# Kernel optimization log

Measured on AMD Instinct MI355X. Metric: run time of the kernel, lower is better.

Reference implementation:

```python
import jax, jax.numpy as jnp
import numpy as np
from jax import lax

B, L, D, H, OM = 16, 512, 2048, 512, 5


def _lstm(seq, wih, whh, bih, bhh):
    # seq: [T, B, F]; PyTorch gate order i, f, g, o
    Hh = whh.shape[1]
    Bb = seq.shape[1]
    def step(carry, xt):
        h, c = carry
        g = xt @ wih.T + h @ whh.T + bih + bhh
        i, f, gg, o = jnp.split(g, 4, axis=-1)
        c = jax.nn.sigmoid(f) * c + jax.nn.sigmoid(i) * jnp.tanh(gg)
        h = jax.nn.sigmoid(o) * jnp.tanh(c)
        return (h, c), h
    z = jnp.zeros((Bb, Hh), seq.dtype)
    _, hs = lax.scan(step, (z, z), seq)
    return hs  # [T, B, Hh]


def setup_inputs() -> dict:
    key = jax.random.key(0)
    ks = jax.random.split(key, 17)
    s = 0.02
    f32 = jnp.float32
    inp = {
        "x": jax.random.normal(ks[0], (B, L, D), f32),
        "wb": jax.random.normal(ks[1], (H, D, OM), f32) * s,
        "bb": jax.random.normal(ks[2], (H,), f32) * s,
        "wa": jax.random.normal(ks[3], (H, D, OM), f32) * s,
        "ba": jax.random.normal(ks[4], (H,), f32) * s,
        "wr": jax.random.normal(ks[5], (H, D, 2 * OM), f32) * s,
        "br": jax.random.normal(ks[6], (H,), f32) * s,
        "wih_f": jax.random.normal(ks[7], (4 * H, H + 1), f32) * s,
        "whh_f": jax.random.normal(ks[8], (4 * H, H), f32) * s,
        "bih_f": jax.random.normal(ks[9], (4 * H,), f32) * s,
        "bhh_f": jax.random.normal(ks[10], (4 * H,), f32) * s,
        "wih_r": jax.random.normal(ks[11], (4 * H, H + 1), f32) * s,
        "whh_r": jax.random.normal(ks[12], (4 * H, H), f32) * s,
        "bih_r": jax.random.normal(ks[13], (4 * H,), f32) * s,
        "bhh_r": jax.random.normal(ks[14], (4 * H,), f32) * s,
        "wfc": jax.random.normal(ks[15], (1, 2 * H), f32) * s,
        "bfc": jax.random.normal(ks[16], (1,), f32) * s,
    }
    return inp


def reference(x, wb, bb, wa, ba, wr, br, wih_f, whh_f, bih_f, bhh_f,
              wih_r, whh_r, bih_r, bhh_r, wfc, bfc):
    om = OM
    xc = jnp.transpose(x, (0, 2, 1))  # [B, D, L]
    conv = lambda w, b: lax.conv_general_dilated(
        xc, w, (1,), 'VALID', dimension_numbers=('NCH', 'OIH', 'NCH')) + b[None, :, None]
    cb = conv(wb, bb)  # [B, H, L-om+1]
    ca = conv(wa, ba)  # [B, H, L-om+1]
    cr = conv(wr, br)  # [B, H, L-2om+1]
    T = x.shape[1] - 2 * om  # number of centers c in [om, L-om)
    d_before = cb[:, :, 0:T]          # window [c-om, c) == conv output c-om
    d_after = ca[:, :, om:om + T]     # window [c, c+om) == conv output c
    vts_d = jnp.sum(d_before * d_after, axis=1, keepdims=True)  # [B, 1, T]
    vts_r = cr[:, :, 0:T]             # full window; pool over length-1 is identity
    vts_seq = jnp.concatenate([vts_r, vts_d], axis=1)  # [B, H+1, T]
    seq = jnp.transpose(vts_seq, (2, 0, 1))  # [T, B, H+1]
    hs_f = _lstm(seq, wih_f, whh_f, bih_f, bhh_f)
    hs_r = _lstm(seq[::-1], wih_r, whh_r, bih_r, bhh_r)[::-1]
    h = jnp.concatenate([hs_f, hs_r], axis=-1)  # [T, B, 2H]
    logits = jnp.einsum('tbh,h->tb', h, wfc[0]) + bfc[0]
    return jax.nn.sigmoid(jnp.transpose(logits))  # [B, T]
```

## Files before the change

kernel.cpp:

```cpp
#include <hip/hip_runtime.h>
#include <hip/hip_bf16.h>

typedef short v8s __attribute__((ext_vector_type(8)));
typedef float v4f __attribute__((ext_vector_type(4)));
typedef unsigned int u32;
typedef unsigned short u16;
typedef unsigned long long u64;

__device__ __forceinline__ u16 f2bf(float f) {
    union { float f; u32 u; } x; x.f = f;
    u32 r = x.u + 0x7fffu + ((x.u >> 16) & 1u);
    return (u16)(r >> 16);
}
__device__ __forceinline__ float bf2f(u16 s) {
    union { u32 u; float f; } x; x.u = ((u32)s) << 16;
    return x.f;
}
__device__ __forceinline__ float sigmoidf_(float x) { return 1.f / (1.f + __expf(-x)); }
__device__ __forceinline__ float tanh_fast(float x) {
    float t = fminf(fmaxf(x, -15.f), 15.f);
    float e = __expf(2.f * t);
    return (e - 1.f) / (e + 1.f);
}

__global__ __launch_bounds__(256) void xbf_kernel(const float* __restrict__ x, u16* __restrict__ xbf, int n) {
    int i = (blockIdx.x * 256 + threadIdx.x) * 4;
    if (i + 3 < n) {
        float4 v = *(const float4*)(x + i);
        u16* d = xbf + i;
        d[0] = f2bf(v.x); d[1] = f2bf(v.y); d[2] = f2bf(v.z); d[3] = f2bf(v.w);
    }
}

__global__ __launch_bounds__(256) void packw_kernel(const float* __restrict__ wb, const float* __restrict__ wa,
                                                    const float* __restrict__ wr, u16* __restrict__ W1, u16* __restrict__ W2) {
    long idx = (long)blockIdx.x * 256 + threadIdx.x;
    int which = idx >= (1024L * 10240) ? 1 : 0;
    long rem = idx - (long)which * 1024 * 10240;
    int n = (int)(rem / 10240);
    int kap = (int)(rem % 10240);
    int tap = kap >> 11, d = kap & 2047;
    float v;
    if (n < 512) v = which ? wa[(long)n * 10240 + d * 5 + tap] : wb[(long)n * 10240 + d * 5 + tap];
    else         v = wr[(long)(n - 512) * 20480 + d * 10 + tap + (which ? 5 : 0)];
    (which ? W2 : W1)[rem] = f2bf(v);
}

__global__ __launch_bounds__(256) void packwih_kernel(const float* __restrict__ wf, const float* __restrict__ wr,
                                                      u16* __restrict__ Bp) {
    int idx = blockIdx.x * 256 + threadIdx.x;
    int n = idx / 576, kap = idx % 576;
    int dir = n >> 11, g = n & 2047;
    const float* src = dir ? wr : wf;
    float v = (kap < 513) ? src[(long)g * 513 + kap] : 0.f;
    Bp[idx] = f2bf(v);
}

__global__ __launch_bounds__(256) void packwhh_kernel(const float* __restrict__ whf, const float* __restrict__ whr,
                                                      u16* __restrict__ W) {
    int idx = blockIdx.x * 256 + threadIdx.x;
    int dir = idx >> 20;
    float v = dir ? whr[idx & 1048575] : whf[idx];
    W[idx] = f2bf(v);
}

__global__ __launch_bounds__(256) void misc_kernel(const float* __restrict__ bihf, const float* __restrict__ bhhf,
                                                   const float* __restrict__ bihr, const float* __restrict__ bhhr,
                                                   float* __restrict__ bsum, u64* __restrict__ hbuf) {
    int i = blockIdx.x * 256 + threadIdx.x;
    if (i < 2048) bsum[i] = bihf[i] + bhhf[i];
    else if (i < 4096) bsum[i] = bihr[i - 2048] + bhhr[i - 2048];
    else if (i < 4096 + 16384) hbuf[i - 4096] = 0xFFFFFFFF00000000ULL;
}

template <int OUTBF>
__global__ __launch_bounds__(256) void gemm_bf16(const u16* __restrict__ A, const u16* __restrict__ B,
                                                 void* __restrict__ Cv, int M, int N, int K, int ldc,
                                                 int row_div, u32 row_mul1, u32 row_mul2, u32 row_base) {
    __shared__ u16 ldsA[128 * 64];
    __shared__ u16 ldsB[128 * 64];
    const int ntn = N >> 7;
    const int nwg = gridDim.x;
    const int bid = blockIdx.x;
    const int swz = (bid & 7) * (nwg >> 3) + (bid >> 3);
    const int tm = swz / ntn, tn = swz % ntn;
    const int tid = threadIdx.x, lane = tid & 63, wv = tid >> 6;
    const int wm = wv >> 1, wn = wv & 1;
    const int qbase = wv * 4;

    u32 asrc[4], bsrc[4];
#pragma unroll
    for (int it = 0; it < 4; ++it) {
        int q = qbase + it;
        int r = q * 8 + (lane >> 3);
        int cb = ((lane & 7) * 16) ^ ((r & 7) << 4);
        int m = tm * 128 + r; if (m > M - 1) m = M - 1;
        asrc[it] = row_base + (u32)(m / row_div) * row_mul1 + (u32)(m % row_div) * row_mul2 + (u32)(cb >> 1);
        int n = tn * 128 + r;
        bsrc[it] = (u32)n * (u32)K + (u32)(cb >> 1);
    }

    v4f acc[4][4];
#pragma unroll
    for (int i = 0; i < 4; ++i)
#pragma unroll
        for (int j = 0; j < 4; ++j) acc[i][j] = (v4f){0.f, 0.f, 0.f, 0.f};

    const int KT = K >> 6;
    for (int kt = 0; kt < KT; ++kt) {
        const int k0 = kt << 6;
#pragma unroll
        for (int it = 0; it < 4; ++it) {
            int q = qbase + it;
            __builtin_amdgcn_global_load_lds(
                (const __attribute__((address_space(1))) u32*)(A + asrc[it] + k0),
                (__attribute__((address_space(3))) u32*)((char*)ldsA + q * 1024), 16, 0, 0);
            __builtin_amdgcn_global_load_lds(
                (const __attribute__((address_space(1))) u32*)(B + bsrc[it] + k0),
                (__attribute__((address_space(3))) u32*)((char*)ldsB + q * 1024), 16, 0, 0);
        }
        __syncthreads();
#pragma unroll
        for (int kk = 0; kk < 2; ++kk) {
            v8s af[4], bfr[4];
#pragma unroll
            for (int i = 0; i < 4; ++i) {
                int row = wm * 64 + i * 16 + (lane & 15);
                int cbyte = (kk * 64 + ((lane >> 4) * 16)) ^ ((row & 7) << 4);
                af[i] = *(const v8s*)((const char*)ldsA + row * 128 + cbyte);
                int rn = wn * 64 + i * 16 + (lane & 15);
                int cbn = (kk * 64 + ((lane >> 4) * 16)) ^ ((rn & 7) << 4);
                bfr[i] = *(const v8s*)((const char*)ldsB + rn * 128 + cbn);
            }
#pragma unroll
            for (int i = 0; i < 4; ++i)
#pragma unroll
                for (int j = 0; j < 4; ++j)
                    acc[i][j] = __builtin_amdgcn_mfma_f32_16x16x32_bf16(af[i], bfr[j], acc[i][j], 0, 0, 0);
        }
        __syncthreads();
    }
#pragma unroll
    for (int i = 0; i < 4; ++i)
#pragma unroll
        for (int j = 0; j < 4; ++j)
#pragma unroll
            for (int r = 0; r < 4; ++r) {
                int m = tm * 128 + wm * 64 + i * 16 + (lane >> 4) * 4 + r;
                int n = tn * 128 + wn * 64 + j * 16 + (lane & 15);
                if (m < M) {
                    if (OUTBF) ((u16*)Cv)[(long)m * ldc + n] = f2bf(acc[i][j][r]);
                    else       ((float*)Cv)[(long)m * ldc + n] = acc[i][j][r];
                }
            }
}

__global__ __launch_bounds__(256) void combine_kernel(const float* __restrict__ G1, const float* __restrict__ G2,
                                                      const float* __restrict__ bb, const float* __restrict__ ba,
                                                      const float* __restrict__ br, u16* __restrict__ seqpad) {
    int m = blockIdx.x;
    int b = m / 502, t = m % 502;
    int tid = threadIdx.x;
    const float* g1 = G1 + (long)m * 1024;
    const float* g2 = G2 + (long)m * 1024;
    u16* dst = seqpad + (long)(t * 16 + b) * 576;
    float part = 0.f;
#pragma unroll
    for (int rep = 0; rep < 2; ++rep) {
        int u = tid + rep * 256;
        float db = g1[u] + bb[u];
        float da = g2[u] + ba[u];
        part += db * da;
        float vr = g1[512 + u] + g2[512 + u] + br[u];
        dst[u] = f2bf(vr);
    }
#pragma unroll
    for (int off = 32; off; off >>= 1) part += __shfl_down(part, off, 64);
    __shared__ float red[4];
    if ((tid & 63) == 0) red[tid >> 6] = part;
    __syncthreads();
    if (tid == 0) dst[512] = f2bf(red[0] + red[1] + red[2] + red[3]);
    if (tid >= 1 && tid < 64) dst[512 + tid] = 0;
}

__global__ __launch_bounds__(256, 1) void lstm_kernel(const u16* __restrict__ P, const u16* __restrict__ whhbf,
                                                      const float* __restrict__ bsum, u64* hbuf,
                                                      u16* __restrict__ hs) {
    const int wg = blockIdx.x;
    const int dir = wg >> 4, j = wg & 15;
    const int tid = threadIdx.x, lane = tid & 63, w = tid >> 6;
    __shared__ u16 hls[16 * 512];
    __shared__ float gls[4][16][32];

    v8s bf[2][16];
    const u16* whd = whhbf + (long)dir * 2048 * 512;
#pragma unroll
    for (int nt = 0; nt < 2; ++nt) {
        int n = w * 512 + j * 32 + nt * 16 + (lane & 15);
#pragma unroll
        for (int kt = 0; kt < 16; ++kt)
            bf[nt][kt] = *(const v8s*)(whd + (long)n * 512 + kt * 32 + ((lane >> 4) * 8));
    }

    for (int i = tid; i < 8192; i += 256) hls[i] = 0;

    const int b_ = tid >> 4;
    const int u_ = (tid * 2) & 31;
    float c0 = 0.f, c1 = 0.f;
    u64* hb = hbuf + dir * 2 * 4096;
    const int col0 = w * 512 + j * 32 + (lane & 15);
    const float bs0 = bsum[dir * 2048 + col0];
    const float bs1 = bsum[dir * 2048 + col0 + 16];
    const u16* Pd = P + dir * 2048;

    float pv[2][4];
    {
        int tau = dir ? 501 : 0;
#pragma unroll
        for (int nt = 0; nt < 2; ++nt)
#pragma unroll
            for (int r = 0; r < 4; ++r)
                pv[nt][r] = bf2f(Pd[(long)(tau * 16 + ((lane >> 4) * 4 + r)) * 4096 + col0 + nt * 16]);
    }
    __syncthreads();

    for (int s = 0; s < 502; ++s) {
        const int tau = dir ? (501 - s) : s;
        if (s > 0) {
            const u64* slot = hb + ((s - 1) & 1) * 4096;
            const u32 want = (u32)(s - 1);
            u64 vv[16];
            for (;;) {
                u32 ok = 0;
#pragma unroll
                for (int rep = 0; rep < 16; ++rep)
                    vv[rep] = __hip_atomic_load(slot + tid + rep * 256, __ATOMIC_RELAXED, __HIP_MEMORY_SCOPE_AGENT);
#pragma unroll
                for (int rep = 0; rep < 16; ++rep)
                    ok += ((u32)(vv[rep] >> 32) == want);
                if (ok == 16) break;
            }
#pragma unroll
            for (int rep = 0; rep < 16; ++rep) {
                int i_ = tid + rep * 256;
                int bb_ = i_ >> 8;
                int bo_ = (bb_ << 10) + (((i_ & 255) << 2) ^ ((bb_ & 7) << 4));
                *(u32*)((char*)hls + bo_) = (u32)vv[rep];
            }
        }
        __syncthreads();
        v4f a0a, a1a, a0b = (v4f){0, 0, 0, 0}, a1b = (v4f){0, 0, 0, 0};
#pragma unroll
        for (int r = 0; r < 4; ++r) { a0a[r] = pv[0][r] + bs0; a1a[r] = pv[1][r] + bs1; }
#pragma unroll
        for (int kt = 0; kt < 16; kt += 2) {
            int row = lane & 15;
            int cb0 = (kt * 64 + ((lane >> 4) * 16)) ^ ((row & 7) << 4);
            int cb1 = ((kt + 1) * 64 + ((lane >> 4) * 16)) ^ ((row & 7) << 4);
            v8s af0 = *(const v8s*)((const char*)hls + row * 1024 + cb0);
            v8s af1 = *(const v8s*)((const char*)hls + row * 1024 + cb1);
            a0a = __builtin_amdgcn_mfma_f32_16x16x32_bf16(af0, bf[0][kt], a0a, 0, 0, 0);
            a1a = __builtin_amdgcn_mfma_f32_16x16x32_bf16(af0, bf[1][kt], a1a, 0, 0, 0);
            a0b = __builtin_amdgcn_mfma_f32_16x16x32_bf16(af1, bf[0][kt + 1], a0b, 0, 0, 0);
            a1b = __builtin_amdgcn_mfma_f32_16x16x32_bf16(af1, bf[1][kt + 1], a1b, 0, 0, 0);
        }
#pragma unroll
        for (int r = 0; r < 4; ++r) {
            gls[w][(lane >> 4) * 4 + r][(lane & 15)] = a0a[r] + a0b[r];
            gls[w][(lane >> 4) * 4 + r][16 + (lane & 15)] = a1a[r] + a1b[r];
        }
        __syncthreads();
        float i0 = gls[0][b_][u_],     f0 = gls[1][b_][u_],     g0 = gls[2][b_][u_],     o0 = gls[3][b_][u_];
        float i1 = gls[0][b_][u_ + 1], f1 = gls[1][b_][u_ + 1], g1v = gls[2][b_][u_ + 1], o1 = gls[3][b_][u_ + 1];
        c0 = sigmoidf_(f0) * c0 + sigmoidf_(i0) * tanh_fast(g0);
        c1 = sigmoidf_(f1) * c1 + sigmoidf_(i1) * tanh_fast(g1v);
        float h0 = sigmoidf_(o0) * tanh_fast(c0);
        float h1 = sigmoidf_(o1) * tanh_fast(c1);
        u32 hw = (u32)f2bf(h0) | ((u32)f2bf(h1) << 16);
        int gi = (b_ * 512 + j * 32 + u_) >> 1;
        __hip_atomic_store(hb + (s & 1) * 4096 + gi, (u64)hw | ((u64)(u32)s << 32),
                           __ATOMIC_RELAXED, __HIP_MEMORY_SCOPE_AGENT);
        *(u32*)(hs + (((long)(dir * 502 + tau) * 16 + b_) * 512 + j * 32 + u_)) = hw;
        if (s + 1 < 502) {
            int tau2 = dir ? (500 - s) : (s + 1);
#pragma unroll
            for (int nt = 0; nt < 2; ++nt)
#pragma unroll
                for (int r = 0; r < 4; ++r)
                    pv[nt][r] = bf2f(Pd[(long)(tau2 * 16 + ((lane >> 4) * 4 + r)) * 4096 + col0 + nt * 16]);
        }
    }
}

__global__ __launch_bounds__(256) void final_kernel(const u16* __restrict__ hs, const float* __restrict__ wfc,
                                                    const float* __restrict__ bfc, float* __restrict__ out) {
    int m = blockIdx.x;
    int t = m >> 4, b = m & 15;
    int tid = threadIdx.x;
    const u16* hf = hs + ((long)t * 16 + b) * 512;
    const u16* hr = hs + ((long)(502 + t) * 16 + b) * 512;
    float part = 0.f;
#pragma unroll
    for (int rep = 0; rep < 2; ++rep) {
        int u = tid + rep * 256;
        part += bf2f(hf[u]) * wfc[u] + bf2f(hr[u]) * wfc[512 + u];
    }
#pragma unroll
    for (int off = 32; off; off >>= 1) part += __shfl_down(part, off, 64);
    __shared__ float red[4];
    if ((tid & 63) == 0) red[tid >> 6] = part;
    __syncthreads();
    if (tid == 0) {
        float lg = red[0] + red[1] + red[2] + red[3] + bfc[0];
        out[(long)b * 502 + t] = 1.f / (1.f + __expf(-lg));
    }
}

extern "C" void kernel_launch(void* const* d_in, const int* in_sizes, int n_in,
                              void* d_out, int out_size, void* d_ws, size_t ws_size,
                              hipStream_t stream) {
    const float* x     = (const float*)d_in[0];
    const float* wb    = (const float*)d_in[1];
    const float* bb    = (const float*)d_in[2];
    const float* wa    = (const float*)d_in[3];
    const float* ba    = (const float*)d_in[4];
    const float* wr    = (const float*)d_in[5];
    const float* br    = (const float*)d_in[6];
    const float* wih_f = (const float*)d_in[7];
    const float* whh_f = (const float*)d_in[8];
    const float* bih_f = (const float*)d_in[9];
    const float* bhh_f = (const float*)d_in[10];
    const float* wih_r = (const float*)d_in[11];
    const float* whh_r = (const float*)d_in[12];
    const float* bih_r = (const float*)d_in[13];
    const float* bhh_r = (const float*)d_in[14];
    const float* wfc   = (const float*)d_in[15];
    const float* bfc   = (const float*)d_in[16];
    float* out = (float*)d_out;

    char* ws = (char*)d_ws;
    u16* xbf = (u16*)ws;
    u16* W1  = (u16*)(ws + 33554432);
    u16* W2  = (u16*)(ws + 54525952);
    u16* Pb  = (u16*)ws;
    char* r2 = ws + 75497472;
    float* G1 = (float*)r2;
    float* G2 = (float*)(r2 + 32899072);
    u16*  hs  = (u16*)r2;
    char* r3 = r2 + 65798144;
    u16*  seqp = (u16*)r3;
    u16*  wihp = (u16*)(r3 + 9252864);
    u16*  whhb = (u16*)(r3 + 13971456);
    float* bsum= (float*)(r3 + 18165760);
    u64*  hbuf = (u64*)(r3 + 18182144);

    xbf_kernel<<<16384, 256, 0, stream>>>(x, xbf, 16 * 512 * 2048);
    packw_kernel<<<81920, 256, 0, stream>>>(wb, wa, wr, W1, W2);
    packwih_kernel<<<9216, 256, 0, stream>>>(wih_f, wih_r, wihp);
    packwhh_kernel<<<8192, 256, 0, stream>>>(whh_f, whh_r, whhb);
    misc_kernel<<<80, 256, 0, stream>>>(bih_f, bhh_f, bih_r, bhh_r, bsum, hbuf);

    gemm_bf16<0><<<63 * 8, 256, 0, stream>>>(xbf, W1, G1, 8032, 1024, 10240, 1024,
                                             502, 512u * 2048u, 2048u, 0u);
    gemm_bf16<0><<<63 * 8, 256, 0, stream>>>(xbf, W2, G2, 8032, 1024, 10240, 1024,
                                             502, 512u * 2048u, 2048u, 5u * 2048u);
    combine_kernel<<<8032, 256, 0, stream>>>(G1, G2, bb, ba, br, seqp);
    gemm_bf16<1><<<63 * 32, 256, 0, stream>>>(seqp, wihp, Pb, 8032, 4096, 576, 4096,
                                              8032, 0u, 576u, 0u);
    lstm_kernel<<<32, 256, 0, stream>>>(Pb, whhb, bsum, hbuf, hs);
    final_kernel<<<8032, 256, 0, stream>>>(hs, wfc, bfc, out);
}
```

Measured before the change: 1.803 ms.

## Merge conv GEMMs into 128x256-tile kernel, vectorize weight pack and LSTM polling

The two conv GEMM launches become one kernel whose blocks each compute a 128x256 tile, so every A tile loaded into LDS feeds twice as many MFMAs. The weight pack kernel now writes four bf16 values per thread with a single 8-byte store. The LSTM hidden-state poll replaces sixteen 8-byte atomic loads per thread with eight inline-asm dwordx4 loads using sc1. The larger tile doubles accumulator registers, which may lower occupancy, and the asm poll depends on sc1 cache semantics being enough for visibility across blocks.

```diff
diff --git a/kernel.cpp b/kernel.cpp
--- a/kernel.cpp
+++ b/kernel.cpp
@@ -4,6 +4,7 @@
 typedef short v8s __attribute__((ext_vector_type(8)));
 typedef float v4f __attribute__((ext_vector_type(4)));
 typedef unsigned int u32;
+typedef unsigned int u32x4 __attribute__((ext_vector_type(4)));
 typedef unsigned short u16;
 typedef unsigned long long u64;
 
@@ -34,16 +35,23 @@
 
 __global__ __launch_bounds__(256) void packw_kernel(const float* __restrict__ wb, const float* __restrict__ wa,
                                                     const float* __restrict__ wr, u16* __restrict__ W1, u16* __restrict__ W2) {
-    long idx = (long)blockIdx.x * 256 + threadIdx.x;
-    int which = idx >= (1024L * 10240) ? 1 : 0;
-    long rem = idx - (long)which * 1024 * 10240;
+    long e = ((long)blockIdx.x * 256 + threadIdx.x) * 4;
+    int which = e >= (1024L * 10240) ? 1 : 0;
+    long rem = e - (long)which * 1024 * 10240;
     int n = (int)(rem / 10240);
     int kap = (int)(rem % 10240);
     int tap = kap >> 11, d = kap & 2047;
-    float v;
-    if (n < 512) v = which ? wa[(long)n * 10240 + d * 5 + tap] : wb[(long)n * 10240 + d * 5 + tap];
-    else         v = wr[(long)(n - 512) * 20480 + d * 10 + tap + (which ? 5 : 0)];
-    (which ? W2 : W1)[rem] = f2bf(v);
+    u16 o[4];
+    if (n < 512) {
+        const float* src = which ? wa : wb;
+#pragma unroll
+        for (int q = 0; q < 4; ++q) o[q] = f2bf(src[(long)n * 10240 + (d + q) * 5 + tap]);
+    } else {
+        const float* src = wr + (long)(n - 512) * 20480 + tap + (which ? 5 : 0);
+#pragma unroll
+        for (int q = 0; q < 4; ++q) o[q] = f2bf(src[(d + q) * 10]);
+    }
+    *(u64*)((which ? W2 : W1) + rem) = *(const u64*)o;
 }
 
 __global__ __launch_bounds__(256) void packwih_kernel(const float* __restrict__ wf, const float* __restrict__ wr,
@@ -73,10 +81,104 @@
     else if (i < 4096 + 16384) hbuf[i - 4096] = 0xFFFFFFFF00000000ULL;
 }
 
-template <int OUTBF>
+__global__ __launch_bounds__(256) void gemm_conv(const u16* __restrict__ A, const u16* __restrict__ W1,
+                                                 const u16* __restrict__ W2, float* __restrict__ G1,
+                                                 float* __restrict__ G2) {
+    __shared__ u16 ldsA[128 * 64];
+    __shared__ u16 ldsB[256 * 64];
+    const int M = 8032, K = 10240;
+    const int bid = blockIdx.x;
+    const int swz = (bid & 7) * 63 + (bid >> 3);
+    const int sel = swz >= 252 ? 1 : 0;
+    const int rem = swz - sel * 252;
+    const int tm = rem >> 2, tn2 = rem & 3;
+    const u16* B = sel ? W2 : W1;
+    float* C = sel ? G2 : G1;
+    const u32 row_base = sel ? 10240u : 0u;
+    const int tid = threadIdx.x, lane = tid & 63, wv = tid >> 6;
+    const int wm = wv >> 1, wn = wv & 1;
+
+    u32 asrc[4], bsrc[8];
+#pragma unroll
+    for (int it = 0; it < 4; ++it) {
+        int q = wv * 4 + it;
+        int r = q * 8 + (lane >> 3);
+        int cb = ((lane & 7) * 16) ^ ((r & 7) << 4);
+        int m = tm * 128 + r; if (m > M - 1) m = M - 1;
+        asrc[it] = row_base + (u32)(m / 502) * (512u * 2048u) + (u32)(m % 502) * 2048u + (u32)(cb >> 1);
+    }
+#pragma unroll
+    for (int it = 0; it < 8; ++it) {
+        int qb = wv * 8 + it;
+        int r2 = qb * 8 + (lane >> 3);
+        int cb = ((lane & 7) * 16) ^ ((r2 & 7) << 4);
+        int n = tn2 * 256 + r2;
+        bsrc[it] = (u32)n * (u32)K + (u32)(cb >> 1);
+    }
+
+    v4f acc0[4][4], acc1[4][4];
+#pragma unroll
+    for (int i = 0; i < 4; ++i)
+#pragma unroll
+        for (int j = 0; j < 4; ++j) { acc0[i][j] = (v4f){0,0,0,0}; acc1[i][j] = (v4f){0,0,0,0}; }
+
+    for (int kt = 0; kt < 160; ++kt) {
+        const int k0 = kt << 6;
+#pragma unroll
+        for (int it = 0; it < 4; ++it) {
+            __builtin_amdgcn_global_load_lds(
+                (const __attribute__((address_space(1))) u32*)(A + asrc[it] + k0),
+                (__attribute__((address_space(3))) u32*)((char*)ldsA + (wv * 4 + it) * 1024), 16, 0, 0);
+        }
+#pragma unroll
+        for (int it = 0; it < 8; ++it) {
+            __builtin_amdgcn_global_load_lds(
+                (const __attribute__((address_space(1))) u32*)(B + bsrc[it] + k0),
+                (__attribute__((address_space(3))) u32*)((char*)ldsB + (wv * 8 + it) * 1024), 16, 0, 0);
+        }
+        __syncthreads();
+#pragma unroll
+        for (int kk = 0; kk < 2; ++kk) {
+            v8s af[4], b0[4], b1[4];
+#pragma unroll
+            for (int i = 0; i < 4; ++i) {
+                int row = wm * 64 + i * 16 + (lane & 15);
+                int cbyte = (kk * 64 + ((lane >> 4) * 16)) ^ ((row & 7) << 4);
+                af[i] = *(const v8s*)((const char*)ldsA + row * 128 + cbyte);
+                int rn = wn * 64 + i * 16 + (lane & 15);
+                int cbn = (kk * 64 + ((lane >> 4) * 16)) ^ ((rn & 7) << 4);
+                b0[i] = *(const v8s*)((const char*)ldsB + rn * 128 + cbn);
+                int rn1 = 128 + rn;
+                int cbn1 = (kk * 64 + ((lane >> 4) * 16)) ^ ((rn1 & 7) << 4);
+                b1[i] = *(const v8s*)((const char*)ldsB + rn1 * 128 + cbn1);
+            }
+#pragma unroll
+            for (int i = 0; i < 4; ++i)
+#pragma unroll
+                for (int j = 0; j < 4; ++j) {
+                    acc0[i][j] = __builtin_amdgcn_mfma_f32_16x16x32_bf16(af[i], b0[j], acc0[i][j], 0, 0, 0);
+                    acc1[i][j] = __builtin_amdgcn_mfma_f32_16x16x32_bf16(af[i], b1[j], acc1[i][j], 0, 0, 0);
+                }
+        }
+        __syncthreads();
+    }
+#pragma unroll
+    for (int i = 0; i < 4; ++i)
+#pragma unroll
+        for (int j = 0; j < 4; ++j)
+#pragma unroll
+            for (int r = 0; r < 4; ++r) {
+                int m = tm * 128 + wm * 64 + i * 16 + (lane >> 4) * 4 + r;
+                if (m < M) {
+                    int c0 = tn2 * 256 + wn * 64 + j * 16 + (lane & 15);
+                    C[(long)m * 1024 + c0] = acc0[i][j][r];
+                    C[(long)m * 1024 + c0 + 128] = acc1[i][j][r];
+                }
+            }
+}
+
 __global__ __launch_bounds__(256) void gemm_bf16(const u16* __restrict__ A, const u16* __restrict__ B,
-                                                 void* __restrict__ Cv, int M, int N, int K, int ldc,
-                                                 int row_div, u32 row_mul1, u32 row_mul2, u32 row_base) {
+                                                 u16* __restrict__ Cv, int M, int N, int K, int ldc) {
     __shared__ u16 ldsA[128 * 64];
     __shared__ u16 ldsB[128 * 64];
     const int ntn = N >> 7;
@@ -95,7 +197,7 @@
         int r = q * 8 + (lane >> 3);
         int cb = ((lane & 7) * 16) ^ ((r & 7) << 4);
         int m = tm * 128 + r; if (m > M - 1) m = M - 1;
-        asrc[it] = row_base + (u32)(m / row_div) * row_mul1 + (u32)(m % row_div) * row_mul2 + (u32)(cb >> 1);
+        asrc[it] = (u32)m * (u32)K + (u32)(cb >> 1);
         int n = tn * 128 + r;
         bsrc[it] = (u32)n * (u32)K + (u32)(cb >> 1);
     }
@@ -148,10 +250,7 @@
             for (int r = 0; r < 4; ++r) {
                 int m = tm * 128 + wm * 64 + i * 16 + (lane >> 4) * 4 + r;
                 int n = tn * 128 + wn * 64 + j * 16 + (lane & 15);
-                if (m < M) {
-                    if (OUTBF) ((u16*)Cv)[(long)m * ldc + n] = f2bf(acc[i][j][r]);
-                    else       ((float*)Cv)[(long)m * ldc + n] = acc[i][j][r];
-                }
+                if (m < M) Cv[(long)m * ldc + n] = f2bf(acc[i][j][r]);
             }
 }
 
@@ -227,26 +326,45 @@
     for (int s = 0; s < 502; ++s) {
         const int tau = dir ? (501 - s) : s;
         if (s > 0) {
-            const u64* slot = hb + ((s - 1) & 1) * 4096;
+            const u64* slotp = hb + ((s - 1) & 1) * 4096;
             const u32 want = (u32)(s - 1);
-            u64 vv[16];
+            u64 base = (u64)slotp + (u64)tid * 16;
+            u64 a0 = base,          a1 = base + 4096,  a2 = base + 8192,  a3 = base + 12288;
+            u64 a4 = base + 16384,  a5 = base + 20480, a6 = base + 24576, a7 = base + 28672;
+            u32x4 w0, w1, w2, w3, w4, w5, w6, w7;
             for (;;) {
-                u32 ok = 0;
-#pragma unroll
-                for (int rep = 0; rep < 16; ++rep)
-                    vv[rep] = __hip_atomic_load(slot + tid + rep * 256, __ATOMIC_RELAXED, __HIP_MEMORY_SCOPE_AGENT);
-#pragma unroll
-                for (int rep = 0; rep < 16; ++rep)
-                    ok += ((u32)(vv[rep] >> 32) == want);
+                asm volatile(
+                    "global_load_dwordx4 %[w0], %[a0], off sc1\n\t"
+                    "global_load_dwordx4 %[w1], %[a1], off sc1\n\t"
+                    "global_load_dwordx4 %[w2], %[a2], off sc1\n\t"
+                    "global_load_dwordx4 %[w3], %[a3], off sc1\n\t"
+                    "global_load_dwordx4 %[w4], %[a4], off sc1\n\t"
+                    "global_load_dwordx4 %[w5], %[a5], off sc1\n\t"
+                    "global_load_dwordx4 %[w6], %[a6], off sc1\n\t"
+                    "global_load_dwordx4 %[w7], %[a7], off sc1\n\t"
+                    "s_waitcnt vmcnt(0)"
+                    : [w0]"=v"(w0), [w1]"=v"(w1), [w2]"=v"(w2), [w3]"=v"(w3),
+                      [w4]"=v"(w4), [w5]"=v"(w5), [w6]"=v"(w6), [w7]"=v"(w7)
+                    : [a0]"v"(a0), [a1]"v"(a1), [a2]"v"(a2), [a3]"v"(a3),
+                      [a4]"v"(a4), [a5]"v"(a5), [a6]"v"(a6), [a7]"v"(a7)
+                    : "memory");
+                u32 ok = (w0[1] == want) + (w0[3] == want) + (w1[1] == want) + (w1[3] == want)
+                       + (w2[1] == want) + (w2[3] == want) + (w3[1] == want) + (w3[3] == want)
+                       + (w4[1] == want) + (w4[3] == want) + (w5[1] == want) + (w5[3] == want)
+                       + (w6[1] == want) + (w6[3] == want) + (w7[1] == want) + (w7[3] == want);
                 if (ok == 16) break;
             }
-#pragma unroll
-            for (int rep = 0; rep < 16; ++rep) {
-                int i_ = tid + rep * 256;
-                int bb_ = i_ >> 8;
-                int bo_ = (bb_ << 10) + (((i_ & 255) << 2) ^ ((bb_ & 7) << 4));
-                *(u32*)((char*)hls + bo_) = (u32)vv[rep];
-            }
+#define FILL(rep, pay0, pay1) {                                                             \
+            int i0 = tid * 2 + (rep) * 512;                                                 \
+            int bb2 = i0 >> 8; int p = i0 & 255;                                            \
+            int bo = (bb2 << 10) + ((p << 2) ^ ((bb2 & 7) << 4));                           \
+            *(u32*)((char*)hls + bo) = (pay0);                                              \
+            int i1 = i0 + 1; int p1 = i1 & 255;                                             \
+            int bo1 = (bb2 << 10) + ((p1 << 2) ^ ((bb2 & 7) << 4));                         \
+            *(u32*)((char*)hls + bo1) = (pay1); }
+            FILL(0, w0[0], w0[2]) FILL(1, w1[0], w1[2]) FILL(2, w2[0], w2[2]) FILL(3, w3[0], w3[2])
+            FILL(4, w4[0], w4[2]) FILL(5, w5[0], w5[2]) FILL(6, w6[0], w6[2]) FILL(7, w7[0], w7[2])
+#undef FILL
         }
         __syncthreads();
         v4f a0a, a1a, a0b = (v4f){0, 0, 0, 0}, a1b = (v4f){0, 0, 0, 0};
@@ -355,18 +473,14 @@
     u64*  hbuf = (u64*)(r3 + 18182144);
 
     xbf_kernel<<<16384, 256, 0, stream>>>(x, xbf, 16 * 512 * 2048);
-    packw_kernel<<<81920, 256, 0, stream>>>(wb, wa, wr, W1, W2);
+    packw_kernel<<<20480, 256, 0, stream>>>(wb, wa, wr, W1, W2);
     packwih_kernel<<<9216, 256, 0, stream>>>(wih_f, wih_r, wihp);
     packwhh_kernel<<<8192, 256, 0, stream>>>(whh_f, whh_r, whhb);
     misc_kernel<<<80, 256, 0, stream>>>(bih_f, bhh_f, bih_r, bhh_r, bsum, hbuf);
 
-    gemm_bf16<0><<<63 * 8, 256, 0, stream>>>(xbf, W1, G1, 8032, 1024, 10240, 1024,
-                                             502, 512u * 2048u, 2048u, 0u);
-    gemm_bf16<0><<<63 * 8, 256, 0, stream>>>(xbf, W2, G2, 8032, 1024, 10240, 1024,
-                                             502, 512u * 2048u, 2048u, 5u * 2048u);
+    gemm_conv<<<504, 256, 0, stream>>>(xbf, W1, W2, G1, G2);
     combine_kernel<<<8032, 256, 0, stream>>>(G1, G2, bb, ba, br, seqp);
-    gemm_bf16<1><<<63 * 32, 256, 0, stream>>>(seqp, wihp, Pb, 8032, 4096, 576, 4096,
-                                              8032, 0u, 576u, 0u);
+    gemm_bf16<<<63 * 32, 256, 0, stream>>>(seqp, wihp, Pb, 8032, 4096, 576, 4096);
     lstm_kernel<<<32, 256, 0, stream>>>(Pb, whhb, bsum, hbuf, hs);
     final_kernel<<<8032, 256, 0, stream>>>(hs, wfc, bfc, out);
 }
```

New measurement: 1.874 ms. 3.9% more time.
